# Optimization experiments

Measured on AMD Instinct MI355X. Metric: run time of the kernel, lower is better.

## Reference

```python
import jax, jax.numpy as jnp
import numpy as np
import math

B, S, F, R = 16, 2048, 512, 4
EPS = 1e-5

def setup_inputs() -> dict:
    key = jax.random.key(0)
    ks = jax.random.split(key, 8)
    s = 1.0 / math.sqrt(S)
    return {
        "x": jax.random.normal(ks[0], (B, S, F), dtype=jnp.float32),
        "Wq": jax.random.uniform(ks[1], (R, S), jnp.float32, -s, s),
        "bq": jnp.zeros((R,), jnp.float32),
        "Wk": jax.random.uniform(ks[2], (R, S), jnp.float32, -s, s),
        "bk": jnp.zeros((R,), jnp.float32),
        "Wv": jax.random.uniform(ks[3], (S, S), jnp.float32, -s, s),
        "bv": jnp.zeros((S,), jnp.float32),
        "ln_w": jnp.ones((S, F), jnp.float32),
        "ln_b": jnp.zeros((S, F), jnp.float32),
        "alpha": jnp.asarray(0.1, jnp.float32),
        "beta": jnp.asarray(0.1, jnp.float32),
    }

def reference(x, Wq, bq, Wk, bk, Wv, bv, ln_w, ln_b, alpha, beta):
    # LayerNorm over last two dims [S, F]
    mu = jnp.mean(x, axis=(1, 2), keepdims=True)
    var = jnp.mean(jnp.square(x - mu), axis=(1, 2), keepdims=True)
    x_norm = (x - mu) * jax.lax.rsqrt(var + EPS) * ln_w + ln_b
    x_t = jnp.swapaxes(x_norm, 1, 2)  # [B, F, S]
    Q = jnp.einsum('bfs,rs->bfr', x_t, Wq) + bq  # [B, F, R]
    K = jnp.einsum('bfs,rs->bfr', x_t, Wk) + bk  # [B, F, R]
    A = jnp.einsum('bfr,bgr->bfg', Q, K) / math.sqrt(R)  # [B, F, F]
    A = jax.nn.softmax(A, axis=-1)
    V = jnp.einsum('bfs,ts->bft', x_t, Wv) + bv  # [B, F, S]
    out = jnp.einsum('bfg,bgs->bfs', A, V)  # [B, F, S]
    # dropout in eval mode = identity
    out = x_t + alpha * out + V + beta * V
    return jnp.swapaxes(out, 1, 2)  # [B, S, F]
```

## Files before the change

### kernel.cpp

```cpp
#include <hip/hip_runtime.h>
#include <hip/hip_bf16.h>

#define NB 16
#define SS 2048
#define FF 512

typedef __bf16 bf16_t;
typedef __bf16 bf16x8 __attribute__((ext_vector_type(8)));
typedef __bf16 bf16x4 __attribute__((ext_vector_type(4)));
typedef float  f32x4  __attribute__((ext_vector_type(4)));

__global__ __launch_bounds__(256) void stats_kernel(const float* __restrict__ x,
                                                    float* __restrict__ partials) {
    const int b = blockIdx.y;
    const float* xb = x + ((size_t)b << 20) + (size_t)blockIdx.x * 16384;
    float s = 0.0f, ss = 0.0f;
#pragma unroll
    for (int i = 0; i < 16; ++i) {
        const float4 v = *(const float4*)&xb[(threadIdx.x + i * 256) * 4];
        s  += v.x + v.y + v.z + v.w;
        ss += v.x * v.x + v.y * v.y + v.z * v.z + v.w * v.w;
    }
#pragma unroll
    for (int off = 32; off > 0; off >>= 1) {
        s  += __shfl_down(s, off);
        ss += __shfl_down(ss, off);
    }
    __shared__ float ps[4], pss[4];
    const int w = threadIdx.x >> 6, lane = threadIdx.x & 63;
    if (lane == 0) { ps[w] = s; pss[w] = ss; }
    __syncthreads();
    if (threadIdx.x == 0) {
        partials[b * 64 + blockIdx.x]        = ps[0] + ps[1] + ps[2] + ps[3];
        partials[1024 + b * 64 + blockIdx.x] = pss[0] + pss[1] + pss[2] + pss[3];
    }
}

__global__ __launch_bounds__(256) void finalize_stats(const float* __restrict__ partials,
                                                      float* __restrict__ musig) {
    const int tid = threadIdx.x;
    const int b = tid >> 4, i = tid & 15;
    float s = 0.f, ss = 0.f;
#pragma unroll
    for (int j = 0; j < 4; ++j) {
        s  += partials[b * 64 + i * 4 + j];
        ss += partials[1024 + b * 64 + i * 4 + j];
    }
#pragma unroll
    for (int off = 8; off > 0; off >>= 1) {
        s  += __shfl_xor(s, off);
        ss += __shfl_xor(ss, off);
    }
    if (i == 0) {
        const float inv_n = 1.0f / 1048576.0f;
        const float mu  = s * inv_n;
        const float var = ss * inv_n - mu * mu;
        musig[b]      = mu;
        musig[16 + b] = rsqrtf(var + 1e-5f);
    }
}

__global__ __launch_bounds__(256) void ynorm_kernel(const float* __restrict__ x,
                                                    const float* __restrict__ lw,
                                                    const float* __restrict__ lb,
                                                    const float* __restrict__ musig,
                                                    bf16_t* __restrict__ Y,
                                                    bf16_t* __restrict__ Xn) {
    __shared__ bf16_t t[32][36];
    const int b = blockIdx.z;
    const int f0 = blockIdx.x * 32, s0 = blockIdx.y * 32;
    const float mu = musig[b], rs = musig[16 + b];
    const int tid = threadIdx.x;
    {
        const int s_loc = tid >> 3, c4 = (tid & 7) * 4;
        const size_t idx = (size_t)(s0 + s_loc) * FF + f0 + c4;
        const float4 xv = *(const float4*)&x[((size_t)b << 20) + idx];
        const float4 wv = *(const float4*)&lw[idx];
        const float4 bv = *(const float4*)&lb[idx];
        bf16x4 o;
        o[0] = (bf16_t)((xv.x - mu) * rs * wv.x + bv.x);
        o[1] = (bf16_t)((xv.y - mu) * rs * wv.y + bv.y);
        o[2] = (bf16_t)((xv.z - mu) * rs * wv.z + bv.z);
        o[3] = (bf16_t)((xv.w - mu) * rs * wv.w + bv.w);
        t[s_loc][c4 + 0] = o[0];
        t[s_loc][c4 + 1] = o[1];
        t[s_loc][c4 + 2] = o[2];
        t[s_loc][c4 + 3] = o[3];
        if (Xn) *(bf16x4*)&Xn[((size_t)b << 20) + idx] = o;
    }
    __syncthreads();
    {
        const int f_loc = tid >> 3, s4 = (tid & 7) * 4;
        bf16x4 o;
        o[0] = t[s4 + 0][f_loc];
        o[1] = t[s4 + 1][f_loc];
        o[2] = t[s4 + 2][f_loc];
        o[3] = t[s4 + 3][f_loc];
        *(bf16x4*)&Y[((size_t)b << 20) + (size_t)(f0 + f_loc) * SS + s0 + s4] = o;
    }
}

__global__ __launch_bounds__(256) void cast_wv(const float* __restrict__ Wv,
                                               bf16_t* __restrict__ Wvb) {
    const size_t i = ((size_t)blockIdx.x * 256 + threadIdx.x) * 4;
    const float4 v = *(const float4*)&Wv[i];
    bf16x4 o;
    o[0] = (bf16_t)v.x; o[1] = (bf16_t)v.y; o[2] = (bf16_t)v.z; o[3] = (bf16_t)v.w;
    *(bf16x4*)&Wvb[i] = o;
}

__global__ __launch_bounds__(256) void qk_kernel(const bf16_t* __restrict__ Y,
                                                 const float* __restrict__ Wq,
                                                 const float* __restrict__ bq,
                                                 const float* __restrict__ Wk,
                                                 const float* __restrict__ bk,
                                                 float* __restrict__ Qo,
                                                 float* __restrict__ Ko) {
    const int w = threadIdx.x >> 6, lane = threadIdx.x & 63;
    const int row = blockIdx.x * 4 + w;
    const bf16_t* y = Y + (size_t)row * SS;
    float qa[4] = {0.f, 0.f, 0.f, 0.f}, ka[4] = {0.f, 0.f, 0.f, 0.f};
#pragma unroll
    for (int c = 0; c < 4; ++c) {
        const int s = c * 512 + lane * 8;
        const bf16x8 yv = *(const bf16x8*)&y[s];
        float yf[8];
#pragma unroll
        for (int j = 0; j < 8; ++j) yf[j] = (float)yv[j];
#pragma unroll
        for (int r = 0; r < 4; ++r) {
            const float4 a0 = *(const float4*)&Wq[r * SS + s];
            const float4 a1 = *(const float4*)&Wq[r * SS + s + 4];
            const float4 c0 = *(const float4*)&Wk[r * SS + s];
            const float4 c1 = *(const float4*)&Wk[r * SS + s + 4];
            qa[r] += yf[0]*a0.x + yf[1]*a0.y + yf[2]*a0.z + yf[3]*a0.w
                   + yf[4]*a1.x + yf[5]*a1.y + yf[6]*a1.z + yf[7]*a1.w;
            ka[r] += yf[0]*c0.x + yf[1]*c0.y + yf[2]*c0.z + yf[3]*c0.w
                   + yf[4]*c1.x + yf[5]*c1.y + yf[6]*c1.z + yf[7]*c1.w;
        }
    }
#pragma unroll
    for (int off = 32; off > 0; off >>= 1) {
#pragma unroll
        for (int r = 0; r < 4; ++r) {
            qa[r] += __shfl_down(qa[r], off);
            ka[r] += __shfl_down(ka[r], off);
        }
    }
    if (lane == 0) {
#pragma unroll
        for (int r = 0; r < 4; ++r) {
            Qo[(size_t)row * 4 + r] = qa[r] + bq[r];
            Ko[(size_t)row * 4 + r] = ka[r] + bk[r];
        }
    }
}

__global__ __launch_bounds__(256) void softmax_kernel(const float* __restrict__ Qo,
                                                      const float* __restrict__ Ko,
                                                      bf16_t* __restrict__ Aout) {
    const int w = threadIdx.x >> 6, lane = threadIdx.x & 63;
    const int row = blockIdx.x * 4 + w;
    const int b = row >> 9;
    const float4 q = *(const float4*)&Qo[(size_t)row * 4];
    const float* kb = Ko + (size_t)b * FF * 4;
    float sc[8];
#pragma unroll
    for (int j = 0; j < 8; ++j) {
        const float4 kv = *(const float4*)&kb[(lane * 8 + j) * 4];
        sc[j] = (q.x*kv.x + q.y*kv.y + q.z*kv.z + q.w*kv.w) * 0.5f;
    }
    float mx = sc[0];
#pragma unroll
    for (int j = 1; j < 8; ++j) mx = fmaxf(mx, sc[j]);
#pragma unroll
    for (int off = 32; off > 0; off >>= 1) mx = fmaxf(mx, __shfl_xor(mx, off));
    float sum = 0.f;
#pragma unroll
    for (int j = 0; j < 8; ++j) { sc[j] = __expf(sc[j] - mx); sum += sc[j]; }
#pragma unroll
    for (int off = 32; off > 0; off >>= 1) sum += __shfl_xor(sum, off);
    const float inv = 1.0f / sum;
    bf16x8 o;
#pragma unroll
    for (int j = 0; j < 8; ++j) o[j] = (bf16_t)(sc[j] * inv);
    *(bf16x8*)&Aout[(size_t)row * FF + lane * 8] = o;
}

template<int EPI>
__device__ __forceinline__ void gemm_impl(
        const bf16_t* __restrict__ Abase, long long strideA, int lda,
        const bf16_t* __restrict__ Bbase, long long strideB, int ldb,
        bf16_t* __restrict__ Cbase, long long strideC, int ldc,
        int NTILES, const float* __restrict__ bias_m,
        const float* __restrict__ xp, const float* __restrict__ lwp,
        const float* __restrict__ lbp, const bf16_t* __restrict__ xnp,
        const float* __restrict__ musig,
        const float* __restrict__ alphap, const float* __restrict__ betap,
        float* __restrict__ outp) {
    __shared__ __align__(16) bf16_t As[2][16384];
    __shared__ __align__(16) bf16_t Bs[2][16384];
    const int tid = threadIdx.x;
    const int w = tid >> 6, lane = tid & 63;

    const int nchunk = gridDim.x >> 3;
    const int wgid = (blockIdx.x & 7) * nchunk + (blockIdx.x >> 3);
    const int bz = wgid >> 4;
    const int rem = wgid & 15;
    const int m0 = (rem & 7) * 256, n0 = (rem >> 3) * 256;

    const bf16_t* A = Abase + (size_t)bz * (size_t)strideA;
    const bf16_t* B = Bbase + (size_t)bz * (size_t)strideB;
    bf16_t* C = Cbase + (size_t)bz * (size_t)strideC;
    const int wm = w >> 2, wn = w & 3;

    const int rr0 = (w * 2 + 0) * 16 + (lane >> 2);
    const int rr1 = (w * 2 + 1) * 16 + (lane >> 2);
    const int sw0 = ((lane & 3) ^ ((rr0 >> 1) & 3)) * 8;
    const int sw1 = ((lane & 3) ^ ((rr1 >> 1) & 3)) * 8;
    const bf16_t* gA0 = A + (size_t)(m0 + rr0) * lda + sw0;
    const bf16_t* gA1 = A + (size_t)(m0 + rr1) * lda + sw1;
    const bf16_t* gB0 = B + (size_t)(n0 + rr0) * ldb + sw0;
    const bf16_t* gB1 = B + (size_t)(n0 + rr1) * ldb + sw1;
    const int d0 = (w * 2 + 0) * 512;
    const int d1 = (w * 2 + 1) * 512;

#define STA(bi, h, ko) do {                                                          \
    __builtin_amdgcn_global_load_lds(                                                \
        (const __attribute__((address_space(1))) unsigned int*)(gA0 + (ko) + (h)*32),\
        (__attribute__((address_space(3))) unsigned int*)&As[bi][(h)*8192 + d0], 16, 0, 0); \
    __builtin_amdgcn_global_load_lds(                                                \
        (const __attribute__((address_space(1))) unsigned int*)(gA1 + (ko) + (h)*32),\
        (__attribute__((address_space(3))) unsigned int*)&As[bi][(h)*8192 + d1], 16, 0, 0); \
} while (0)
#define STB(bi, h, ko) do {                                                          \
    __builtin_amdgcn_global_load_lds(                                                \
        (const __attribute__((address_space(1))) unsigned int*)(gB0 + (ko) + (h)*32),\
        (__attribute__((address_space(3))) unsigned int*)&Bs[bi][(h)*8192 + d0], 16, 0, 0); \
    __builtin_amdgcn_global_load_lds(                                                \
        (const __attribute__((address_space(1))) unsigned int*)(gB1 + (ko) + (h)*32),\
        (__attribute__((address_space(3))) unsigned int*)&Bs[bi][(h)*8192 + d1], 16, 0, 0); \
} while (0)

    const int cs = lane >> 4;
    int offA[2][8], offB[2][4];
#pragma unroll
    for (int kk = 0; kk < 2; ++kk) {
#pragma unroll
        for (int mt = 0; mt < 8; ++mt) {
            const int r = wm * 128 + mt * 16 + (lane & 15);
            offA[kk][mt] = kk * 8192 + r * 32 + ((cs ^ ((r >> 1) & 3)) << 3);
        }
#pragma unroll
        for (int nt = 0; nt < 4; ++nt) {
            const int r = wn * 64 + nt * 16 + (lane & 15);
            offB[kk][nt] = kk * 8192 + r * 32 + ((cs ^ ((r >> 1) & 3)) << 3);
        }
    }

#define RD_A(dst, base, kk, mh) do { _Pragma("unroll")                        \
    for (int i = 0; i < 4; ++i) dst[i] = *(const bf16x8*)&(base)[offA[kk][(mh)*4 + i]]; } while (0)
#define RD_B(dst, base, kk) do { _Pragma("unroll")                            \
    for (int i = 0; i < 4; ++i) dst[i] = *(const bf16x8*)&(base)[offB[kk][i]]; } while (0)
#define MFMA16X(af, bfr, mh) do { _Pragma("unroll")                           \
    for (int i = 0; i < 4; ++i) { _Pragma("unroll")                           \
        for (int nt = 0; nt < 4; ++nt)                                        \
            acc[(mh)*4 + i][nt] = __builtin_amdgcn_mfma_f32_16x16x32_bf16(    \
                af[i], bfr[nt], acc[(mh)*4 + i][nt], 0, 0, 0); } } while (0)
#define VMC(n) asm volatile("s_waitcnt vmcnt(" #n ")" ::: "memory")
#define HBAR  __builtin_amdgcn_s_barrier()
#define LGKM(n) do { asm volatile("s_waitcnt lgkmcnt(" #n ")" ::: "memory");  \
                     __builtin_amdgcn_sched_barrier(0); } while (0)
#define SBAR  __builtin_amdgcn_sched_barrier(0)
#define PRIO1 __builtin_amdgcn_s_setprio(1)
#define PRIO0 __builtin_amdgcn_s_setprio(0)

    f32x4 acc[8][4] = {};
    bf16x8 afA[4], afB[4], bfrA[4], bfrB[4];
    const int mask = NTILES - 1;

    STA(0, 0, 0); STB(0, 0, 0); STA(0, 1, 0); STB(0, 1, 0);
    VMC(4); HBAR;
    RD_A(afA, As[0], 0, 0); RD_B(bfrA, Bs[0], 0);

    for (int t = 0; t < NTILES; ++t) {
        const int cur = t & 1, oth = cur ^ 1;
        const int ko = ((t + 1) & mask) * 64;
        const bf16_t* as  = As[cur];
        const bf16_t* bs  = Bs[cur];
        const bf16_t* asn = As[oth];
        const bf16_t* bsn = Bs[oth];
        RD_A(afB, as, 0, 1); SBAR;
        STA(oth, 0, ko); SBAR;
        LGKM(4);
        PRIO1; MFMA16X(afA, bfrA, 0); PRIO0; SBAR;
        VMC(2); HBAR;
        RD_A(afA, as, 1, 0); RD_B(bfrB, bs, 1); SBAR;
        STB(oth, 0, ko); SBAR;
        LGKM(8);
        PRIO1; MFMA16X(afB, bfrA, 1); PRIO0; SBAR;
        RD_A(afB, as, 1, 1); SBAR;
        STA(oth, 1, ko); SBAR;
        LGKM(4);
        PRIO1; MFMA16X(afA, bfrB, 0); PRIO0; SBAR;
        VMC(2); HBAR;
        RD_A(afA, asn, 0, 0); RD_B(bfrA, bsn, 0); SBAR;
        STB(oth, 1, ko); SBAR;
        LGKM(8);
        PRIO1; MFMA16X(afB, bfrB, 1); PRIO0; SBAR;
    }
#undef STA
#undef STB
#undef RD_A
#undef RD_B
#undef MFMA16X
#undef VMC
#undef HBAR
#undef LGKM
#undef SBAR
#undef PRIO1
#undef PRIO0

    if constexpr (EPI == 0) {
#pragma unroll
        for (int mt = 0; mt < 8; ++mt) {
#pragma unroll
            for (int r = 0; r < 4; ++r) {
                const int row = m0 + wm * 128 + mt * 16 + ((lane >> 4) << 2) + r;
                const float bm = bias_m ? bias_m[row] : 0.0f;
#pragma unroll
                for (int nt = 0; nt < 4; ++nt) {
                    const int col = n0 + wn * 64 + nt * 16 + (lane & 15);
                    C[(size_t)row * ldc + col] = (bf16_t)(acc[mt][nt][r] + bm);
                }
            }
        }
    } else {
        asm volatile("s_waitcnt vmcnt(0) lgkmcnt(0)" ::: "memory");
        __syncthreads();
        float* lsc0 = (float*)&As[0][0];
        float* lsc1 = (float*)&As[1][0];
        const float alpha = alphap[0];
        const float onepb = 1.0f + betap[0];
        float mu = 0.f, rs = 0.f;
        if constexpr (EPI == 1) { mu = musig[bz]; rs = musig[16 + bz]; }
        const float* xb = (EPI == 1) ? xp + ((size_t)bz << 20) : nullptr;
        const bf16_t* xnb = (EPI == 2) ? xnp + ((size_t)bz << 20) : nullptr;
        float* ob = outp + ((size_t)bz << 20);
        const int lrow = wm * 16 + ((lane >> 4) << 2);
        const int lcol = wn * 64 + (lane & 15);
        const int gr = tid >> 4;
        const int gc = (tid & 15) * 16;
#define SCAT(mt, bank) do { _Pragma("unroll")                                 \
    for (int r = 0; r < 4; ++r) { _Pragma("unroll")                           \
        for (int nt = 0; nt < 4; ++nt)                                        \
            (bank)[(lrow + r) * 256 + lcol + nt * 16] = acc[mt][nt][r]; } } while (0)
        SCAT(0, lsc0);
        __syncthreads();
#pragma unroll
        for (int mt = 0; mt < 8; ++mt) {
            float* bank  = (mt & 1) ? lsc1 : lsc0;
            float* nbank = (mt & 1) ? lsc0 : lsc1;
            const int grow = m0 + (gr >> 4) * 128 + mt * 16 + (gr & 15);
            const size_t idx = (size_t)grow * FF + n0 + gc;
            const bf16x8 vt0 = *(const bf16x8*)&A[(size_t)grow * lda + n0 + gc];
            const bf16x8 vt1 = *(const bf16x8*)&A[(size_t)grow * lda + n0 + gc + 8];
            bf16x8 xn0, xn1;
            float4 xv[4], wv[4], bv4[4];
            if constexpr (EPI == 2) {
                xn0 = *(const bf16x8*)&xnb[idx];
                xn1 = *(const bf16x8*)&xnb[idx + 8];
            } else {
#pragma unroll
                for (int j = 0; j < 4; ++j) {
                    xv[j]  = *(const float4*)&xb[idx + j * 4];
                    wv[j]  = *(const float4*)&lwp[idx + j * 4];
                    bv4[j] = *(const float4*)&lbp[idx + j * 4];
                }
            }
            if (mt < 7) {
                switch (mt + 1) {
                    case 1: SCAT(1, nbank); break;
                    case 2: SCAT(2, nbank); break;
                    case 3: SCAT(3, nbank); break;
                    case 4: SCAT(4, nbank); break;
                    case 5: SCAT(5, nbank); break;
                    case 6: SCAT(6, nbank); break;
                    case 7: SCAT(7, nbank); break;
                }
            }
#pragma unroll
            for (int j = 0; j < 4; ++j) {
                const float4 av = *(const float4*)&bank[gr * 256 + gc + j * 4];
                float4 o;
                if constexpr (EPI == 2) {
                    const int e = (j & 1) * 4;
                    const bf16x8& xs = (j < 2) ? xn0 : xn1;
                    const bf16x8& vs = (j < 2) ? vt0 : vt1;
                    o.x = (float)xs[e + 0] + alpha * av.x + onepb * (float)vs[e + 0];
                    o.y = (float)xs[e + 1] + alpha * av.y + onepb * (float)vs[e + 1];
                    o.z = (float)xs[e + 2] + alpha * av.z + onepb * (float)vs[e + 2];
                    o.w = (float)xs[e + 3] + alpha * av.w + onepb * (float)vs[e + 3];
                } else {
                    const int e = (j & 1) * 4;
                    const bf16x8& vs = (j < 2) ? vt0 : vt1;
                    o.x = (xv[j].x - mu) * rs * wv[j].x + bv4[j].x + alpha * av.x + onepb * (float)vs[e + 0];
                    o.y = (xv[j].y - mu) * rs * wv[j].y + bv4[j].y + alpha * av.y + onepb * (float)vs[e + 1];
                    o.z = (xv[j].z - mu) * rs * wv[j].z + bv4[j].z + alpha * av.z + onepb * (float)vs[e + 2];
                    o.w = (xv[j].w - mu) * rs * wv[j].w + bv4[j].w + alpha * av.w + onepb * (float)vs[e + 3];
                }
                *(float4*)&ob[idx + j * 4] = o;
            }
            __syncthreads();
        }
#undef SCAT
    }
}

__global__ __launch_bounds__(512, 2) void g1_mm(
        const bf16_t* A, long long sA, int lda, const bf16_t* B, long long sB, int ldb,
        bf16_t* C, long long sC, int ldc, int NT, const float* bias_m) {
    gemm_impl<0>(A, sA, lda, B, sB, ldb, C, sC, ldc, NT, bias_m,
                 nullptr, nullptr, nullptr, nullptr, nullptr, nullptr, nullptr, nullptr);
}

__global__ __launch_bounds__(512, 2) void g2_mm_full(
        const bf16_t* A, long long sA, int lda, const bf16_t* B, long long sB, int ldb,
        int NT, const float* xp, const float* lwp, const float* lbp,
        const float* musig, const float* alphap, const float* betap, float* outp) {
    gemm_impl<1>(A, sA, lda, B, sB, ldb, nullptr, 0, FF, NT, nullptr,
                 xp, lwp, lbp, nullptr, musig, alphap, betap, outp);
}

__global__ __launch_bounds__(512, 2) void g2_mm_lite(
        const bf16_t* A, long long sA, int lda, const bf16_t* B, long long sB, int ldb,
        int NT, const bf16_t* xnp,
        const float* musig, const float* alphap, const float* betap, float* outp) {
    gemm_impl<2>(A, sA, lda, B, sB, ldb, nullptr, 0, FF, NT, nullptr,
                 nullptr, nullptr, nullptr, xnp, musig, alphap, betap, outp);
}

extern "C" void kernel_launch(void* const* d_in, const int* in_sizes, int n_in,
                              void* d_out, int out_size, void* d_ws, size_t ws_size,
                              hipStream_t stream) {
    const float* x   = (const float*)d_in[0];
    const float* Wq  = (const float*)d_in[1];
    const float* bq  = (const float*)d_in[2];
    const float* Wk  = (const float*)d_in[3];
    const float* bk  = (const float*)d_in[4];
    const float* Wv  = (const float*)d_in[5];
    const float* bv  = (const float*)d_in[6];
    const float* lw  = (const float*)d_in[7];
    const float* lb  = (const float*)d_in[8];
    const float* alp = (const float*)d_in[9];
    const float* bet = (const float*)d_in[10];
    float* out = (float*)d_out;

    char* ws = (char*)d_ws;
    float*  musig = (float*)(ws + 128);
    float*  Qo    = (float*)(ws + 256);
    float*  Ko    = (float*)(ws + 256 + 131072);
    bf16_t* Wvb   = (bf16_t*)(ws + 262400);
    bf16_t* Asm   = (bf16_t*)(ws + 8651008);
    float*  partials = (float*)(ws + 8651008);
    bf16_t* Vt    = (bf16_t*)(ws + 17039616);
    bf16_t* Y     = (bf16_t*)(ws + 50594048);
    bf16_t* Xn    = (bf16_t*)(ws + 84148480);
    const bool lite = ws_size >= (size_t)117702912;

    stats_kernel<<<dim3(64, 16), 256, 0, stream>>>(x, partials);
    finalize_stats<<<1, 256, 0, stream>>>(partials, musig);
    cast_wv<<<4096, 256, 0, stream>>>(Wv, Wvb);
    ynorm_kernel<<<dim3(16, 64, 16), 256, 0, stream>>>(x, lw, lb, musig, Y,
                                                       lite ? Xn : (bf16_t*)nullptr);
    qk_kernel<<<2048, 256, 0, stream>>>(Y, Wq, bq, Wk, bk, Qo, Ko);
    softmax_kernel<<<2048, 256, 0, stream>>>(Qo, Ko, Asm);
    g1_mm<<<256, 512, 0, stream>>>(Wvb, 0, SS, Y, 1 << 20, SS, Vt, 1 << 20, FF, 32, bv);
    if (lite) {
        g2_mm_lite<<<256, 512, 0, stream>>>(Vt, 1 << 20, FF, Asm, FF * FF, FF, 8,
                                            Xn, musig, alp, bet, out);
    } else {
        g2_mm_full<<<256, 512, 0, stream>>>(Vt, 1 << 20, FF, Asm, FF * FF, FF, 8,
                                            x, lw, lb, musig, alp, bet, out);
    }
}
```

Baseline: 181.8 us.

## Batch four rows per wave in qk_kernel and issue all GEMM tile loads upfront

qk_kernel now has each wave compute Q/K projections for four rows, so every Wq/Wk load is reused four times and the grid shrinks to 512 blocks. Separately, the GEMM main loop issues all next-tile global-to-LDS stores (A and B halves) at the start of each iteration rather than interleaving them between MFMA groups, with the vmcnt waits adjusted to match. The aim is to cut redundant weight traffic in qk and give global loads more time in flight. The trade-offs are higher register pressure in qk, and in the GEMM more outstanding memory operations plus heavier wait points.

```diff
diff --git a/kernel.cpp b/kernel.cpp
--- a/kernel.cpp
+++ b/kernel.cpp
@@ -117,42 +117,52 @@
                                                  float* __restrict__ Qo,
                                                  float* __restrict__ Ko) {
     const int w = threadIdx.x >> 6, lane = threadIdx.x & 63;
-    const int row = blockIdx.x * 4 + w;
-    const bf16_t* y = Y + (size_t)row * SS;
-    float qa[4] = {0.f, 0.f, 0.f, 0.f}, ka[4] = {0.f, 0.f, 0.f, 0.f};
+    const int row0 = blockIdx.x * 16 + w * 4;
+    const bf16_t* y0 = Y + (size_t)row0 * SS;
+    float qa[4][4] = {}, ka[4][4] = {};
 #pragma unroll
     for (int c = 0; c < 4; ++c) {
         const int s = c * 512 + lane * 8;
-        const bf16x8 yv = *(const bf16x8*)&y[s];
-        float yf[8];
-#pragma unroll
-        for (int j = 0; j < 8; ++j) yf[j] = (float)yv[j];
+        float yf[4][8];
+#pragma unroll
+        for (int rr = 0; rr < 4; ++rr) {
+            const bf16x8 yv = *(const bf16x8*)&y0[(size_t)rr * SS + s];
+#pragma unroll
+            for (int j = 0; j < 8; ++j) yf[rr][j] = (float)yv[j];
+        }
 #pragma unroll
         for (int r = 0; r < 4; ++r) {
             const float4 a0 = *(const float4*)&Wq[r * SS + s];
             const float4 a1 = *(const float4*)&Wq[r * SS + s + 4];
             const float4 c0 = *(const float4*)&Wk[r * SS + s];
             const float4 c1 = *(const float4*)&Wk[r * SS + s + 4];
-            qa[r] += yf[0]*a0.x + yf[1]*a0.y + yf[2]*a0.z + yf[3]*a0.w
-                   + yf[4]*a1.x + yf[5]*a1.y + yf[6]*a1.z + yf[7]*a1.w;
-            ka[r] += yf[0]*c0.x + yf[1]*c0.y + yf[2]*c0.z + yf[3]*c0.w
-                   + yf[4]*c1.x + yf[5]*c1.y + yf[6]*c1.z + yf[7]*c1.w;
+#pragma unroll
+            for (int rr = 0; rr < 4; ++rr) {
+                qa[rr][r] += yf[rr][0]*a0.x + yf[rr][1]*a0.y + yf[rr][2]*a0.z + yf[rr][3]*a0.w
+                           + yf[rr][4]*a1.x + yf[rr][5]*a1.y + yf[rr][6]*a1.z + yf[rr][7]*a1.w;
+                ka[rr][r] += yf[rr][0]*c0.x + yf[rr][1]*c0.y + yf[rr][2]*c0.z + yf[rr][3]*c0.w
+                           + yf[rr][4]*c1.x + yf[rr][5]*c1.y + yf[rr][6]*c1.z + yf[rr][7]*c1.w;
+            }
         }
     }
 #pragma unroll
     for (int off = 32; off > 0; off >>= 1) {
 #pragma unroll
-        for (int r = 0; r < 4; ++r) {
-            qa[r] += __shfl_down(qa[r], off);
-            ka[r] += __shfl_down(ka[r], off);
-        }
+        for (int rr = 0; rr < 4; ++rr)
+#pragma unroll
+            for (int r = 0; r < 4; ++r) {
+                qa[rr][r] += __shfl_down(qa[rr][r], off);
+                ka[rr][r] += __shfl_down(ka[rr][r], off);
+            }
     }
     if (lane == 0) {
 #pragma unroll
-        for (int r = 0; r < 4; ++r) {
-            Qo[(size_t)row * 4 + r] = qa[r] + bq[r];
-            Ko[(size_t)row * 4 + r] = ka[r] + bk[r];
-        }
+        for (int rr = 0; rr < 4; ++rr)
+#pragma unroll
+            for (int r = 0; r < 4; ++r) {
+                Qo[(size_t)(row0 + rr) * 4 + r] = qa[rr][r] + bq[r];
+                Ko[(size_t)(row0 + rr) * 4 + r] = ka[rr][r] + bk[r];
+            }
     }
 }
 
@@ -291,21 +301,18 @@
         const bf16_t* asn = As[oth];
         const bf16_t* bsn = Bs[oth];
         RD_A(afB, as, 0, 1); SBAR;
-        STA(oth, 0, ko); SBAR;
+        STA(oth, 0, ko); STB(oth, 0, ko); STA(oth, 1, ko); STB(oth, 1, ko); SBAR;
         LGKM(4);
         PRIO1; MFMA16X(afA, bfrA, 0); PRIO0; SBAR;
-        VMC(2); HBAR;
+        VMC(8); HBAR;
         RD_A(afA, as, 1, 0); RD_B(bfrB, bs, 1); SBAR;
-        STB(oth, 0, ko); SBAR;
         LGKM(8);
         PRIO1; MFMA16X(afB, bfrA, 1); PRIO0; SBAR;
         RD_A(afB, as, 1, 1); SBAR;
-        STA(oth, 1, ko); SBAR;
         LGKM(4);
         PRIO1; MFMA16X(afA, bfrB, 0); PRIO0; SBAR;
-        VMC(2); HBAR;
+        VMC(4); HBAR;
         RD_A(afA, asn, 0, 0); RD_B(bfrA, bsn, 0); SBAR;
-        STB(oth, 1, ko); SBAR;
         LGKM(8);
         PRIO1; MFMA16X(afB, bfrB, 1); PRIO0; SBAR;
     }
@@ -473,7 +480,7 @@
     cast_wv<<<4096, 256, 0, stream>>>(Wv, Wvb);
     ynorm_kernel<<<dim3(16, 64, 16), 256, 0, stream>>>(x, lw, lb, musig, Y,
                                                        lite ? Xn : (bf16_t*)nullptr);
-    qk_kernel<<<2048, 256, 0, stream>>>(Y, Wq, bq, Wk, bk, Qo, Ko);
+    qk_kernel<<<512, 256, 0, stream>>>(Y, Wq, bq, Wk, bk, Qo, Ko);
     softmax_kernel<<<2048, 256, 0, stream>>>(Qo, Ko, Asm);
     g1_mm<<<256, 512, 0, stream>>>(Wvb, 0, SS, Y, 1 << 20, SS, Vt, 1 << 20, FF, 32, bv);
     if (lite) {
```

New measurement: 180.0 us. No clear change (-1.0%).
